# Performance work log

Hardware: AMD Instinct MI355X
Metric: run time of the kernel (lower is better)

## Reference

```python
import jax, jax.numpy as jnp
import numpy as np

N_NODES = 50000
N_EDGES = 800000
IN_CH = 128
HID = 32
HEADS = 4
LATENT = 64
NEG_SLOPE = 0.2  # PyG GATConv default


def setup_inputs() -> dict:
    key = jax.random.key(0)
    ks = jax.random.split(key, 12)
    HC = HID * HEADS
    inp = {
        "x": jax.random.normal(ks[0], (N_NODES, IN_CH), dtype=jnp.float32),
        "edge_index": jax.random.randint(ks[1], (2, N_EDGES), 0, N_NODES, dtype=jnp.int64),
        # GATConv params
        "W_gat": jax.random.normal(ks[2], (IN_CH, HC), dtype=jnp.float32) / np.sqrt(IN_CH),
        "b_gat": jnp.zeros((HC,), dtype=jnp.float32),
        "att_src": jax.random.normal(ks[3], (HEADS, HID), dtype=jnp.float32) / np.sqrt(HID),
        "att_dst": jax.random.normal(ks[4], (HEADS, HID), dtype=jnp.float32) / np.sqrt(HID),
        # encoder / decoder / output linears
        "W_enc": jax.random.normal(ks[5], (HC, LATENT), dtype=jnp.float32) / np.sqrt(HC),
        "b_enc": jnp.zeros((LATENT,), dtype=jnp.float32),
        "W_dec": jax.random.normal(ks[6], (LATENT, HC), dtype=jnp.float32) / np.sqrt(LATENT),
        "b_dec": jnp.zeros((HC,), dtype=jnp.float32),
        "W_out": jax.random.normal(ks[7], (HC, IN_CH), dtype=jnp.float32) / np.sqrt(HC),
        "b_out": jnp.zeros((IN_CH,), dtype=jnp.float32),
    }
    return inp


def reference(x, edge_index, W_gat, b_gat, att_src, att_dst,
              W_enc, b_enc, W_dec, b_dec, W_out, b_out):
    N = x.shape[0]
    H, C = att_src.shape
    # PyG GATConv adds self-loops by default
    loops = jnp.arange(N, dtype=edge_index.dtype)
    src = jnp.concatenate([edge_index[0], loops])  # message sources (x_j)
    dst = jnp.concatenate([edge_index[1], loops])  # aggregation targets (x_i)

    h = (x @ W_gat).reshape(N, H, C)               # [N,H,C]
    a_src = jnp.einsum('nhc,hc->nh', h, att_src)   # [N,H]
    a_dst = jnp.einsum('nhc,hc->nh', h, att_dst)   # [N,H]

    e = jax.nn.leaky_relu(a_src[src] + a_dst[dst], NEG_SLOPE)  # [E,H]
    # segment softmax over destination nodes (numerically stable)
    e_max = jax.ops.segment_max(e, dst, num_segments=N)
    e_exp = jnp.exp(e - e_max[dst])
    denom = jax.ops.segment_sum(e_exp, dst, num_segments=N)
    alpha = e_exp / (denom[dst] + 1e-16)           # [E,H]

    msg = h[src] * alpha[:, :, None]               # [E,H,C]
    agg = jax.ops.segment_sum(msg, dst, num_segments=N)  # [N,H,C]
    gat_out = agg.reshape(N, H * C) + b_gat        # concat heads + bias

    x1 = jax.nn.elu(gat_out)
    encoded = x1 @ W_enc + b_enc
    decoded = encoded @ W_dec + b_dec
    x2 = jax.nn.elu(decoded)
    return x2 @ W_out + b_out
```

## Files before the change

kernel.cpp:

```cpp
#include <hip/hip_runtime.h>
#include <hip/hip_bf16.h>

#define N_NODES 50000
#define N_EDGES 800000
#define BM 64
#define NBUCK 196
#define CAP 6144
#define CHUNK 8192
#define NB_BUCKET_BLOCKS ((N_EDGES + CHUNK - 1) / CHUNK)
#define REPACK_BLOCKS (2 * N_EDGES / 256)
#define SWZ_BLOCKS 192
#define SWZ_G 32768

typedef _Float16 half4v __attribute__((ext_vector_type(4)));
typedef _Float16 half8  __attribute__((ext_vector_type(8)));
typedef float    float4v __attribute__((ext_vector_type(4)));

__device__ __forceinline__ float elu_f(float v) {
    return (v > 0.f) ? v : (__expf(v) - 1.f);
}

__device__ __forceinline__ unsigned f2bf2(float a, float b) {
    unsigned ua = __float_as_uint(a), ub = __float_as_uint(b);
    ua = (ua + 0x7FFFu + ((ua >> 16) & 1u)) >> 16;
    ub = (ub + 0x7FFFu + ((ub >> 16) & 1u)) >> 16;
    return ua | (ub << 16);
}
__device__ __forceinline__ float2 bf2f2(unsigned u) {
    float2 f;
    f.x = __uint_as_float(u << 16);
    f.y = __uint_as_float(u & 0xFFFF0000u);
    return f;
}

__global__ void k_detect(const unsigned* __restrict__ e_raw, int* __restrict__ flag) {
    __shared__ int nz;
    if (threadIdx.x == 0) nz = 0;
    __syncthreads();
    int cnt = 0;
    for (int i = threadIdx.x; i < 2048; i += 256)
        if (e_raw[2 * i + 1] != 0u) cnt = 1;
    if (cnt) atomicOr(&nz, 1);
    __syncthreads();
    if (threadIdx.x == 0) *flag = (nz == 0) ? 1 : 0;
}

__global__ __launch_bounds__(256) void k_pre(const void* __restrict__ e_raw,
        const int* __restrict__ flag, int* __restrict__ edges,
        const float* __restrict__ We, const float* __restrict__ Wd,
        const float* __restrict__ Wo, const float* __restrict__ Wg,
        _Float16* __restrict__ swz, int* __restrict__ bcursor) {
    const int b = blockIdx.x;
    const int tid = threadIdx.x;
    if (b < REPACK_BLOCKS) {
        int i = b * 256 + tid;
        if (*flag) edges[i] = (int)((const long long*)e_raw)[i];
        else       edges[i] = ((const int*)e_raw)[i];
    } else if (b < REPACK_BLOCKS + SWZ_BLOCKS) {
        int t = (b - REPACK_BLOCKS) * 256 + tid;
        const float* W; int base, N;
        if (t < 8192)       { W = We; base = 0;     N = 64;  }
        else if (t < 16384) { W = Wd; base = 8192;  N = 128; }
        else if (t < 32768) { W = Wo; base = 16384; N = 128; }
        else                { W = Wg; base = SWZ_G; N = 128; }
        int loc = t - base;
        int nnt = N >> 4;
        int frag = loc >> 9, r = loc & 511, lane = r >> 3, j = r & 7;
        int kc = frag / nnt, nt = frag - kc * nnt;
        int k = kc * 32 + ((lane >> 4) << 3) + j;
        int n = nt * 16 + (lane & 15);
        swz[t] = (_Float16)W[k * N + n];
    } else {
        bcursor[tid] = 0;
    }
}

__global__ __launch_bounds__(256) void k_gat_lin(const float* __restrict__ x,
        const _Float16* __restrict__ swz, const float* __restrict__ att_s,
        const float* __restrict__ att_d, unsigned* __restrict__ h_bf,
        float* __restrict__ a_src, float* __restrict__ a_dst) {
    __shared__ _Float16 sx[64 * 128];
    __shared__ float sh[64 * 132];
    const int tid = threadIdx.x;
    const int m0 = blockIdx.x * 64;

#pragma unroll
    for (int i = 0; i < 8; i++) {
        int idx = tid + i * 256;
        int r = idx >> 5, c4 = idx & 31;
        int row = m0 + r; if (row >= N_NODES) row = N_NODES - 1;
        float4 v = ((const float4*)(x + (size_t)row * 128))[c4];
        half4v h;
        h[0] = (_Float16)v.x; h[1] = (_Float16)v.y;
        h[2] = (_Float16)v.z; h[3] = (_Float16)v.w;
        *(half4v*)&sx[r * 128 + c4 * 4] = h;
    }
    __syncthreads();

    const int wave = tid >> 6, lane = tid & 63;
    const int lm = lane & 15, lq = lane >> 4;
    const int wrow = wave * 16;

    {
        float4v acc[8];
#pragma unroll
        for (int nt = 0; nt < 8; nt++) acc[nt] = (float4v){0.f, 0.f, 0.f, 0.f};
#pragma unroll
        for (int kc = 0; kc < 4; kc++) {
            half8 a = *(const half8*)&sx[(wrow + lm) * 128 + kc * 32 + lq * 8];
#pragma unroll
            for (int nt = 0; nt < 8; nt++) {
                half8 b = *(const half8*)&swz[SWZ_G + (kc * 8 + nt) * 512 + lane * 8];
                acc[nt] = __builtin_amdgcn_mfma_f32_16x16x32_f16(a, b, acc[nt], 0, 0, 0);
            }
        }
#pragma unroll
        for (int nt = 0; nt < 8; nt++)
#pragma unroll
            for (int r = 0; r < 4; r++)
                sh[(wrow + lq * 4 + r) * 132 + nt * 16 + lm] = acc[nt][r];
    }
    __syncthreads();

    const int c0 = (tid & 31) * 4;
    const int r0 = (tid >> 5) * 8;
    float4 as4 = *(const float4*)&att_s[c0];
    float4 ad4 = *(const float4*)&att_d[c0];
    const int head = c0 >> 5;

#pragma unroll
    for (int r = 0; r < 8; r++) {
        int row = m0 + r0 + r;
        bool ok = row < N_NODES;
        float4 hv = *(const float4*)&sh[(r0 + r) * 132 + c0];
        if (ok) {
            uint2 p;
            p.x = f2bf2(hv.x, hv.y);
            p.y = f2bf2(hv.z, hv.w);
            *(uint2*)&h_bf[(size_t)row * 64 + (c0 >> 1)] = p;
        }
        float vs = hv.x * as4.x + hv.y * as4.y + hv.z * as4.z + hv.w * as4.w;
        float vd = hv.x * ad4.x + hv.y * ad4.y + hv.z * ad4.z + hv.w * ad4.w;
#pragma unroll
        for (int o = 4; o >= 1; o >>= 1) {
            vs += __shfl_down(vs, o, 8);
            vd += __shfl_down(vd, o, 8);
        }
        if (ok && (tid & 7) == 0) {
            a_src[row * 4 + head] = vs;
            a_dst[row * 4 + head] = vd;
        }
    }
}

__global__ __launch_bounds__(256) void k_bucket(const int* __restrict__ edges,
        int* __restrict__ bcursor, uint2* __restrict__ ebuck) {
    __shared__ int lh[256];
    __shared__ int gbase[256];
    __shared__ int lcur[256];
    const int tid = threadIdx.x;
    const int base = blockIdx.x * CHUNK;

    lh[tid] = 0;
    __syncthreads();
#pragma unroll 4
    for (int j = 0; j < CHUNK / 256; j++) {
        int e = base + j * 256 + tid;
        if (e < N_EDGES) {
            int d = edges[N_EDGES + e];
            atomicAdd(&lh[d >> 8], 1);
        }
    }
    __syncthreads();
    if (lh[tid]) gbase[tid] = atomicAdd(&bcursor[tid], lh[tid]);
    lcur[tid] = 0;
    __syncthreads();
#pragma unroll 4
    for (int j = 0; j < CHUNK / 256; j++) {
        int e = base + j * 256 + tid;
        if (e < N_EDGES) {
            int sN = edges[e];
            int d  = edges[N_EDGES + e];
            int b  = d >> 8;
            int idx = gbase[b] + atomicAdd(&lcur[b], 1);
            if (idx < CAP) {
                uint2 pr; pr.x = (unsigned)sN; pr.y = (unsigned)d;
                ebuck[b * CAP + idx] = pr;
            }
        }
    }
}

__global__ __launch_bounds__(256) void k_bfill(const uint2* __restrict__ ebuck,
        const int* __restrict__ bcursor, int2* __restrict__ nodeoff,
        int* __restrict__ csr_src) {
    __shared__ int lh[256];
    __shared__ int lexc[256];
    __shared__ int lcur[256];
    const int tid = threadIdx.x;
    const int b = blockIdx.x;
    const int lo = b * CAP;
    int cnt = bcursor[b]; if (cnt > CAP) cnt = CAP;
    const int hi = lo + cnt;
    const int n0 = b << 8;

    lh[tid] = 0;
    lcur[tid] = 0;
    __syncthreads();
    for (int i = lo + tid; i < hi; i += 256)
        atomicAdd(&lh[ebuck[i].y & 255], 1);
    __syncthreads();
    {
        int v = lh[tid];
        lexc[tid] = v;
        __syncthreads();
        for (int o = 1; o < 256; o <<= 1) {
            int u = (tid >= o) ? lexc[tid - o] : 0;
            __syncthreads();
            lexc[tid] += u;
            __syncthreads();
        }
        int s = lexc[tid] - v;
        __syncthreads();
        lexc[tid] = s;
        int node = n0 + tid;
        if (node < N_NODES) {
            int2 no; no.x = lo + s; no.y = v;
            nodeoff[node] = no;
        }
    }
    __syncthreads();
    for (int i = lo + tid; i < hi; i += 256) {
        uint2 pr = ebuck[i];
        int li = (int)(pr.y & 255);
        int p = atomicAdd(&lcur[li], 1);
        csr_src[lo + lexc[li] + p] = (int)pr.x;
    }
}

__global__ __launch_bounds__(256) void k_gather(const int2* __restrict__ nodeoff,
        const int* __restrict__ csr_src, const float* __restrict__ a_src,
        const float* __restrict__ a_dst, const unsigned* __restrict__ h_bf,
        float* __restrict__ agg) {
    int d = blockIdx.x * 4 + (threadIdx.x >> 6);
    if (d >= N_NODES) return;
    const int lane = threadIdx.x & 63;
    const int half = lane >> 5;
    const int l32 = lane & 31;
    const int hd = l32 >> 3;
    int2 nd = nodeoff[d];
    const int lo = nd.x, hi = nd.x + nd.y;

    const float adh = a_dst[d * 4 + hd];

    float den = 0.f;
    float ax = 0.f, ay = 0.f, az = 0.f, aw = 0.f;

    if (half == 0) {
        float t = a_src[d * 4 + hd] + adh;
        t = t > 0.f ? t : 0.2f * t;
        float es = __expf(t);
        den = es;
        uint2 hu = ((const uint2*)(h_bf + (size_t)d * 64))[l32];
        float2 c01 = bf2f2(hu.x), c23 = bf2f2(hu.y);
        ax = c01.x * es; ay = c01.y * es;
        az = c23.x * es; aw = c23.y * es;
    }

    int base = lo;
    for (; base + 8 <= hi; base += 8) {
        int i0 = base + half;
        int s0 = csr_src[i0 + 0];
        int s1 = csr_src[i0 + 2];
        int s2 = csr_src[i0 + 4];
        int s3 = csr_src[i0 + 6];
        uint2 u0 = ((const uint2*)(h_bf + (size_t)s0 * 64))[l32];
        uint2 u1 = ((const uint2*)(h_bf + (size_t)s1 * 64))[l32];
        uint2 u2 = ((const uint2*)(h_bf + (size_t)s2 * 64))[l32];
        uint2 u3 = ((const uint2*)(h_bf + (size_t)s3 * 64))[l32];
        float a0 = a_src[s0 * 4 + hd];
        float a1 = a_src[s1 * 4 + hd];
        float a2 = a_src[s2 * 4 + hd];
        float a3 = a_src[s3 * 4 + hd];

        float t0 = a0 + adh; t0 = t0 > 0.f ? t0 : 0.2f * t0;
        float t1 = a1 + adh; t1 = t1 > 0.f ? t1 : 0.2f * t1;
        float t2 = a2 + adh; t2 = t2 > 0.f ? t2 : 0.2f * t2;
        float t3 = a3 + adh; t3 = t3 > 0.f ? t3 : 0.2f * t3;
        float e0 = __expf(t0);
        float e1 = __expf(t1);
        float e2 = __expf(t2);
        float e3 = __expf(t3);
        den += (e0 + e1) + (e2 + e3);

        float2 p, q;
        p = bf2f2(u0.x); q = bf2f2(u0.y);
        ax = fmaf(p.x, e0, ax); ay = fmaf(p.y, e0, ay);
        az = fmaf(q.x, e0, az); aw = fmaf(q.y, e0, aw);
        p = bf2f2(u1.x); q = bf2f2(u1.y);
        ax = fmaf(p.x, e1, ax); ay = fmaf(p.y, e1, ay);
        az = fmaf(q.x, e1, az); aw = fmaf(q.y, e1, aw);
        p = bf2f2(u2.x); q = bf2f2(u2.y);
        ax = fmaf(p.x, e2, ax); ay = fmaf(p.y, e2, ay);
        az = fmaf(q.x, e2, az); aw = fmaf(q.y, e2, aw);
        p = bf2f2(u3.x); q = bf2f2(u3.y);
        ax = fmaf(p.x, e3, ax); ay = fmaf(p.y, e3, ay);
        az = fmaf(q.x, e3, az); aw = fmaf(q.y, e3, aw);
    }
    for (int i = base + half; i < hi; i += 2) {
        int s = csr_src[i];
        float tt = a_src[s * 4 + hd] + adh;
        tt = tt > 0.f ? tt : 0.2f * tt;
        float e = __expf(tt);
        den += e;
        uint2 hu = ((const uint2*)(h_bf + (size_t)s * 64))[l32];
        float2 p = bf2f2(hu.x), q = bf2f2(hu.y);
        ax = fmaf(p.x, e, ax); ay = fmaf(p.y, e, ay);
        az = fmaf(q.x, e, az); aw = fmaf(q.y, e, aw);
    }

    den += __shfl_xor(den, 32);
    ax += __shfl_xor(ax, 32);
    ay += __shfl_xor(ay, 32);
    az += __shfl_xor(az, 32);
    aw += __shfl_xor(aw, 32);

    if (half == 0) {
        float inv = 1.f / (den + 1e-16f);
        float4 o; o.x = ax * inv; o.y = ay * inv; o.z = az * inv; o.w = aw * inv;
        ((float4*)(agg + (size_t)d * 128))[l32] = o;
    }
}

__global__ __launch_bounds__(256) void k_mlp(const float* __restrict__ agg,
        const float* __restrict__ b_gat, const _Float16* __restrict__ swz,
        const float* __restrict__ b_enc, const float* __restrict__ b_dec,
        const float* __restrict__ b_out, float* __restrict__ out) {
    __shared__ _Float16 sx[64 * 128];
    __shared__ _Float16 se[4 * 16 * 64];
    const int tid = threadIdx.x;
    const int m0 = blockIdx.x * 64;

#pragma unroll
    for (int i = 0; i < 8; i++) {
        int idx = tid + i * 256;
        int r = idx >> 5, c4 = idx & 31;
        int row = m0 + r; if (row >= N_NODES) row = N_NODES - 1;
        float4 v = ((const float4*)(agg + (size_t)row * 128))[c4];
        float4 bg = ((const float4*)b_gat)[c4];
        half4v h;
        h[0] = (_Float16)elu_f(v.x + bg.x);
        h[1] = (_Float16)elu_f(v.y + bg.y);
        h[2] = (_Float16)elu_f(v.z + bg.z);
        h[3] = (_Float16)elu_f(v.w + bg.w);
        *(half4v*)&sx[r * 128 + c4 * 4] = h;
    }
    __syncthreads();

    const int wave = tid >> 6, lane = tid & 63;
    const int lm = lane & 15, lq = lane >> 4;
    const int wrow = wave * 16;
    _Float16* eslab = &se[wave * 16 * 64];

    {
        float4v acc[4];
#pragma unroll
        for (int nt = 0; nt < 4; nt++) acc[nt] = (float4v){0.f, 0.f, 0.f, 0.f};
#pragma unroll
        for (int kc = 0; kc < 4; kc++) {
            half8 a = *(const half8*)&sx[(wrow + lm) * 128 + kc * 32 + lq * 8];
#pragma unroll
            for (int nt = 0; nt < 4; nt++) {
                half8 b = *(const half8*)&swz[(kc * 4 + nt) * 512 + lane * 8];
                acc[nt] = __builtin_amdgcn_mfma_f32_16x16x32_f16(a, b, acc[nt], 0, 0, 0);
            }
        }
#pragma unroll
        for (int nt = 0; nt < 4; nt++) {
            float be = b_enc[nt * 16 + lm];
#pragma unroll
            for (int r = 0; r < 4; r++)
                eslab[(lq * 4 + r) * 64 + nt * 16 + lm] = (_Float16)(acc[nt][r] + be);
        }
    }

    {
        float4v acc[8];
#pragma unroll
        for (int nt = 0; nt < 8; nt++) acc[nt] = (float4v){0.f, 0.f, 0.f, 0.f};
#pragma unroll
        for (int kc = 0; kc < 2; kc++) {
            half8 a = *(const half8*)&eslab[lm * 64 + kc * 32 + lq * 8];
#pragma unroll
            for (int nt = 0; nt < 8; nt++) {
                half8 b = *(const half8*)&swz[8192 + (kc * 8 + nt) * 512 + lane * 8];
                acc[nt] = __builtin_amdgcn_mfma_f32_16x16x32_f16(a, b, acc[nt], 0, 0, 0);
            }
        }
#pragma unroll
        for (int nt = 0; nt < 8; nt++) {
            float bd = b_dec[nt * 16 + lm];
#pragma unroll
            for (int r = 0; r < 4; r++)
                sx[(wrow + lq * 4 + r) * 128 + nt * 16 + lm] =
                    (_Float16)elu_f(acc[nt][r] + bd);
        }
    }

    {
        float4v acc[8];
#pragma unroll
        for (int nt = 0; nt < 8; nt++) acc[nt] = (float4v){0.f, 0.f, 0.f, 0.f};
#pragma unroll
        for (int kc = 0; kc < 4; kc++) {
            half8 a = *(const half8*)&sx[(wrow + lm) * 128 + kc * 32 + lq * 8];
#pragma unroll
            for (int nt = 0; nt < 8; nt++) {
                half8 b = *(const half8*)&swz[16384 + (kc * 8 + nt) * 512 + lane * 8];
                acc[nt] = __builtin_amdgcn_mfma_f32_16x16x32_f16(a, b, acc[nt], 0, 0, 0);
            }
        }
#pragma unroll
        for (int nt = 0; nt < 8; nt++) {
            float bo = b_out[nt * 16 + lm];
#pragma unroll
            for (int r = 0; r < 4; r++) {
                int row = m0 + wrow + lq * 4 + r;
                if (row < N_NODES)
                    out[(size_t)row * 128 + nt * 16 + lm] = acc[nt][r] + bo;
            }
        }
    }
}

extern "C" void kernel_launch(void* const* d_in, const int* in_sizes, int n_in,
                              void* d_out, int out_size, void* d_ws, size_t ws_size,
                              hipStream_t stream) {
    const float* x       = (const float*)d_in[0];
    const void*  e_raw   = d_in[1];
    const float* W_gat   = (const float*)d_in[2];
    const float* b_gat   = (const float*)d_in[3];
    const float* att_src = (const float*)d_in[4];
    const float* att_dst = (const float*)d_in[5];
    const float* W_enc   = (const float*)d_in[6];
    const float* b_enc   = (const float*)d_in[7];
    const float* W_dec   = (const float*)d_in[8];
    const float* b_dec   = (const float*)d_in[9];
    const float* W_out   = (const float*)d_in[10];
    const float* b_out   = (const float*)d_in[11];
    float* out = (float*)d_out;

    float* ws      = (float*)d_ws;
    float*   hreg  = ws;
    unsigned* h_bf = (unsigned*)hreg;
    float* a_src   = hreg + 6400000;
    float* a_dst   = a_src + 200000;
    float* agg     = a_dst + 200000;
    uint2* ebuck   = (uint2*)agg;
    int*   edges   = (int*)(agg + 6400000);
    int*   csr_src = edges + 1600000;
    int2*  nodeoff = (int2*)(csr_src + NBUCK * CAP);
    int*   flag    = (int*)(nodeoff + 50000);
    int*   bcursor = flag + 1;
    _Float16* swz  = (_Float16*)(((uintptr_t)(bcursor + 256) + 15) & ~(uintptr_t)15);

    const int GBLK = (N_NODES + BM - 1) / BM;

    k_detect<<<1, 256, 0, stream>>>((const unsigned*)e_raw, flag);
    k_pre<<<REPACK_BLOCKS + SWZ_BLOCKS + 1, 256, 0, stream>>>(
        e_raw, flag, edges, W_enc, W_dec, W_out, W_gat, swz, bcursor);

    k_gat_lin<<<GBLK, 256, 0, stream>>>(x, swz, att_src, att_dst, h_bf, a_src, a_dst);

    k_bucket<<<NB_BUCKET_BLOCKS, 256, 0, stream>>>(edges, bcursor, ebuck);
    k_bfill<<<NBUCK, 256, 0, stream>>>(ebuck, bcursor, nodeoff, csr_src);

    k_gather<<<(N_NODES + 3) / 4, 256, 0, stream>>>(nodeoff, csr_src, a_src, a_dst, h_bf, agg);

    k_mlp<<<GBLK, 256, 0, stream>>>(agg, b_gat, swz, b_enc, b_dec, b_out, out);
}
```

Baseline: 213.1 us.

## Drop edge repack pass, fold detection into k_pre, widen bucket fill

Removes the separate edge-index repack to int32 and the standalone detect kernel. k_bucket now reads the raw int64 or int32 edge array directly, based on a flag computed inside k_pre's last block. Bucket chunk size is reduced to give more blocks, and k_bfill runs 1024 threads per block. The goals are to cut one full pass over the edge array, remove a kernel launch, and raise parallelism in the bucketing stages, at the cost of wider int64 reads inside k_bucket.

After: 194.1 us. 1.1x faster.

```diff
diff --git a/kernel.cpp b/kernel.cpp
--- a/kernel.cpp
+++ b/kernel.cpp
@@ -6,14 +6,14 @@
 #define BM 64
 #define NBUCK 196
 #define CAP 6144
-#define CHUNK 8192
+#define CHUNK 2048
 #define NB_BUCKET_BLOCKS ((N_EDGES + CHUNK - 1) / CHUNK)
-#define REPACK_BLOCKS (2 * N_EDGES / 256)
 #define SWZ_BLOCKS 192
 #define SWZ_G 32768
+#define BFT 1024
 
 typedef _Float16 half4v __attribute__((ext_vector_type(4)));
-typedef _Float16 half8  __attribute__((ext_vector_type(8)));
+typedef _Float16 half8 __attribute__((ext_vector_type(8)));
 typedef float    float4v __attribute__((ext_vector_type(4)));
 
 __device__ __forceinline__ float elu_f(float v) {
@@ -33,46 +33,40 @@
     return f;
 }
 
-__global__ void k_detect(const unsigned* __restrict__ e_raw, int* __restrict__ flag) {
-    __shared__ int nz;
-    if (threadIdx.x == 0) nz = 0;
-    __syncthreads();
-    int cnt = 0;
-    for (int i = threadIdx.x; i < 2048; i += 256)
-        if (e_raw[2 * i + 1] != 0u) cnt = 1;
-    if (cnt) atomicOr(&nz, 1);
-    __syncthreads();
-    if (threadIdx.x == 0) *flag = (nz == 0) ? 1 : 0;
-}
-
 __global__ __launch_bounds__(256) void k_pre(const void* __restrict__ e_raw,
-        const int* __restrict__ flag, int* __restrict__ edges,
+        int* __restrict__ flag,
         const float* __restrict__ We, const float* __restrict__ Wd,
         const float* __restrict__ Wo, const float* __restrict__ Wg,
         _Float16* __restrict__ swz, int* __restrict__ bcursor) {
     const int b = blockIdx.x;
     const int tid = threadIdx.x;
-    if (b < REPACK_BLOCKS) {
-        int i = b * 256 + tid;
-        if (*flag) edges[i] = (int)((const long long*)e_raw)[i];
-        else       edges[i] = ((const int*)e_raw)[i];
-    } else if (b < REPACK_BLOCKS + SWZ_BLOCKS) {
-        int t = (b - REPACK_BLOCKS) * 256 + tid;
-        const float* W; int base, N;
-        if (t < 8192)       { W = We; base = 0;     N = 64;  }
-        else if (t < 16384) { W = Wd; base = 8192;  N = 128; }
-        else if (t < 32768) { W = Wo; base = 16384; N = 128; }
-        else                { W = Wg; base = SWZ_G; N = 128; }
-        int loc = t - base;
-        int nnt = N >> 4;
-        int frag = loc >> 9, r = loc & 511, lane = r >> 3, j = r & 7;
-        int kc = frag / nnt, nt = frag - kc * nnt;
-        int k = kc * 32 + ((lane >> 4) << 3) + j;
-        int n = nt * 16 + (lane & 15);
-        swz[t] = (_Float16)W[k * N + n];
-    } else {
+    if (b >= SWZ_BLOCKS) {
+        __shared__ int nz;
+        if (tid == 0) nz = 0;
         bcursor[tid] = 0;
-    }
+        __syncthreads();
+        int cnt = 0;
+        const unsigned* er = (const unsigned*)e_raw;
+        for (int i = tid; i < 2048; i += 256)
+            if (er[2 * i + 1] != 0u) cnt = 1;
+        if (cnt) atomicOr(&nz, 1);
+        __syncthreads();
+        if (tid == 0) *flag = (nz == 0) ? 1 : 0;
+        return;
+    }
+    int t = b * 256 + tid;
+    const float* W; int base, N;
+    if (t < 8192)       { W = We; base = 0;     N = 64;  }
+    else if (t < 16384) { W = Wd; base = 8192;  N = 128; }
+    else if (t < 32768) { W = Wo; base = 16384; N = 128; }
+    else                { W = Wg; base = SWZ_G; N = 128; }
+    int loc = t - base;
+    int nnt = N >> 4;
+    int frag = loc >> 9, r = loc & 511, lane = r >> 3, j = r & 7;
+    int kc = frag / nnt, nt = frag - kc * nnt;
+    int k = kc * 32 + ((lane >> 4) << 3) + j;
+    int n = nt * 16 + (lane & 15);
+    swz[t] = (_Float16)W[k * N + n];
 }
 
 __global__ __launch_bounds__(256) void k_gat_lin(const float* __restrict__ x,
@@ -153,13 +147,17 @@
     }
 }
 
-__global__ __launch_bounds__(256) void k_bucket(const int* __restrict__ edges,
-        int* __restrict__ bcursor, uint2* __restrict__ ebuck) {
+__global__ __launch_bounds__(256) void k_bucket(const void* __restrict__ e_raw,
+        const int* __restrict__ flag, int* __restrict__ bcursor,
+        uint2* __restrict__ ebuck) {
     __shared__ int lh[256];
     __shared__ int gbase[256];
     __shared__ int lcur[256];
     const int tid = threadIdx.x;
     const int base = blockIdx.x * CHUNK;
+    const int is64 = *flag;
+    const long long* e64 = (const long long*)e_raw;
+    const int* e32 = (const int*)e_raw;
 
     lh[tid] = 0;
     __syncthreads();
@@ -167,7 +165,7 @@
     for (int j = 0; j < CHUNK / 256; j++) {
         int e = base + j * 256 + tid;
         if (e < N_EDGES) {
-            int d = edges[N_EDGES + e];
+            int d = is64 ? (int)e64[N_EDGES + e] : e32[N_EDGES + e];
             atomicAdd(&lh[d >> 8], 1);
         }
     }
@@ -179,9 +177,10 @@
     for (int j = 0; j < CHUNK / 256; j++) {
         int e = base + j * 256 + tid;
         if (e < N_EDGES) {
-            int sN = edges[e];
-            int d  = edges[N_EDGES + e];
-            int b  = d >> 8;
+            int sN, d;
+            if (is64) { sN = (int)e64[e]; d = (int)e64[N_EDGES + e]; }
+            else      { sN = e32[e];      d = e32[N_EDGES + e]; }
+            int b = d >> 8;
             int idx = gbase[b] + atomicAdd(&lcur[b], 1);
             if (idx < CAP) {
                 uint2 pr; pr.x = (unsigned)sN; pr.y = (unsigned)d;
@@ -191,7 +190,7 @@
     }
 }
 
-__global__ __launch_bounds__(256) void k_bfill(const uint2* __restrict__ ebuck,
+__global__ __launch_bounds__(BFT) void k_bfill(const uint2* __restrict__ ebuck,
         const int* __restrict__ bcursor, int2* __restrict__ nodeoff,
         int* __restrict__ csr_src) {
     __shared__ int lh[256];
@@ -204,33 +203,33 @@
     const int hi = lo + cnt;
     const int n0 = b << 8;
 
-    lh[tid] = 0;
-    lcur[tid] = 0;
-    __syncthreads();
-    for (int i = lo + tid; i < hi; i += 256)
+    if (tid < 256) { lh[tid] = 0; lcur[tid] = 0; }
+    __syncthreads();
+    for (int i = lo + tid; i < hi; i += BFT)
         atomicAdd(&lh[ebuck[i].y & 255], 1);
     __syncthreads();
     {
-        int v = lh[tid];
-        lexc[tid] = v;
+        int v = 0;
+        if (tid < 256) { v = lh[tid]; lexc[tid] = v; }
         __syncthreads();
         for (int o = 1; o < 256; o <<= 1) {
-            int u = (tid >= o) ? lexc[tid - o] : 0;
+            int u = (tid < 256 && tid >= o) ? lexc[tid - o] : 0;
             __syncthreads();
-            lexc[tid] += u;
+            if (tid < 256) lexc[tid] += u;
             __syncthreads();
         }
-        int s = lexc[tid] - v;
-        __syncthreads();
-        lexc[tid] = s;
-        int node = n0 + tid;
-        if (node < N_NODES) {
-            int2 no; no.x = lo + s; no.y = v;
-            nodeoff[node] = no;
-        }
-    }
-    __syncthreads();
-    for (int i = lo + tid; i < hi; i += 256) {
+        if (tid < 256) {
+            int s = lexc[tid] - v;
+            lexc[tid] = s;
+            int node = n0 + tid;
+            if (node < N_NODES) {
+                int2 no; no.x = lo + s; no.y = v;
+                nodeoff[node] = no;
+            }
+        }
+    }
+    __syncthreads();
+    for (int i = lo + tid; i < hi; i += BFT) {
         uint2 pr = ebuck[i];
         int li = (int)(pr.y & 255);
         int p = atomicAdd(&lcur[li], 1);
@@ -466,14 +465,13 @@
 
     const int GBLK = (N_NODES + BM - 1) / BM;
 
-    k_detect<<<1, 256, 0, stream>>>((const unsigned*)e_raw, flag);
-    k_pre<<<REPACK_BLOCKS + SWZ_BLOCKS + 1, 256, 0, stream>>>(
-        e_raw, flag, edges, W_enc, W_dec, W_out, W_gat, swz, bcursor);
+    k_pre<<<SWZ_BLOCKS + 1, 256, 0, stream>>>(
+        e_raw, flag, W_enc, W_dec, W_out, W_gat, swz, bcursor);
 
     k_gat_lin<<<GBLK, 256, 0, stream>>>(x, swz, att_src, att_dst, h_bf, a_src, a_dst);
 
-    k_bucket<<<NB_BUCKET_BLOCKS, 256, 0, stream>>>(edges, bcursor, ebuck);
-    k_bfill<<<NBUCK, 256, 0, stream>>>(ebuck, bcursor, nodeoff, csr_src);
+    k_bucket<<<NB_BUCKET_BLOCKS, 256, 0, stream>>>(e_raw, flag, bcursor, ebuck);
+    k_bfill<<<NBUCK, BFT, 0, stream>>>(ebuck, bcursor, nodeoff, csr_src);
 
     k_gather<<<(N_NODES + 3) / 4, 256, 0, stream>>>(nodeoff, csr_src, a_src, a_dst, h_bf, agg);
 
```
